# Performance work log

Measured on AMD Instinct MI355X. Metric: run time of the kernel, lower is better.

## Reference

```python
import jax, jax.numpy as jnp
import numpy as np
import math

D_MODEL = 1024
N_HEADS = 8
D_FF = 4 * D_MODEL
EPS = 1e-5


def layer_norm(x, g, b):
    mu = jnp.mean(x, axis=-1, keepdims=True)
    var = jnp.mean(jnp.square(x - mu), axis=-1, keepdims=True)
    return (x - mu) / jnp.sqrt(var + EPS) * g + b


def setup_inputs() -> dict:
    key = jax.random.key(0)
    ks = jax.random.split(key, 8)
    B, S = 1, 4096
    x = jax.random.normal(ks[0], (B, S, D_MODEL), dtype=jnp.float32)
    # linear params (stored as [in, out]); init scale ~ 1/sqrt(fan_in)
    qkv_w = jax.random.normal(ks[1], (D_MODEL, 3 * D_MODEL), dtype=jnp.float32) * (1.0 / math.sqrt(D_MODEL))
    qkv_b = jnp.zeros((3 * D_MODEL,), dtype=jnp.float32)
    w1 = jax.random.normal(ks[2], (D_MODEL, D_FF), dtype=jnp.float32) * (1.0 / math.sqrt(D_MODEL))
    b1 = jnp.zeros((D_FF,), dtype=jnp.float32)
    w2 = jax.random.normal(ks[3], (D_FF, D_MODEL), dtype=jnp.float32) * (1.0 / math.sqrt(D_FF))
    b2 = jnp.zeros((D_MODEL,), dtype=jnp.float32)
    ln1_g = jnp.ones((D_MODEL,), dtype=jnp.float32)
    ln1_b = jnp.zeros((D_MODEL,), dtype=jnp.float32)
    ln2_g = jnp.ones((D_MODEL,), dtype=jnp.float32)
    ln2_b = jnp.zeros((D_MODEL,), dtype=jnp.float32)
    return {"x": x, "ln1_g": ln1_g, "ln1_b": ln1_b, "qkv_w": qkv_w, "qkv_b": qkv_b,
            "ln2_g": ln2_g, "ln2_b": ln2_b, "w1": w1, "b1": b1, "w2": w2, "b2": b2}


def reference(x, ln1_g, ln1_b, qkv_w, qkv_b, ln2_g, ln2_b, w1, b1, w2, b2):
    B, S, D = x.shape
    hd = D // N_HEADS
    scaler = math.sqrt(hd)

    h = layer_norm(x, ln1_g, ln1_b)                       # [B,S,D]
    qkv = h @ qkv_w + qkv_b                               # [B,S,3D]
    q, k, v = jnp.split(qkv, 3, axis=-1)
    # b s (h d) -> b h s d
    def split_heads(t):
        return t.reshape(B, S, N_HEADS, hd).transpose(0, 2, 1, 3)
    q, k, v = split_heads(q), split_heads(k), split_heads(v)
    scores = jnp.einsum('bhqd,bhkd->bhqk', q, k) / scaler  # [B,H,S,S] materialized, as in source
    attn = jax.nn.softmax(scores, axis=-1)
    heads = jnp.einsum('bhqk,bhkd->bhqd', attn, v)        # [B,H,S,hd]
    attn_score = heads.transpose(0, 2, 1, 3).reshape(B, S, D)  # b h t d -> b t (h d)
    # NOTE: source returns attn_score (the proj Linear output is discarded)
    h = attn_score + h                                     # residual with ln1 output
    h = layer_norm(h, ln2_g, ln2_b)
    h = jax.nn.gelu(h @ w1 + b1, approximate=False) @ w2 + b2  # no final residual
    return h
```

## Files before the change

### kernel.cpp

```cpp
#include <hip/hip_runtime.h>
#include <stdint.h>


typedef __bf16 bf16;
typedef __attribute__((ext_vector_type(8))) __bf16 bf16x8;
typedef __attribute__((ext_vector_type(4))) __bf16 bf16x4;
typedef __attribute__((ext_vector_type(4))) float f32x4;

#define DEV static __device__ __forceinline__

#define QSCALE 0.12751741687f

DEV void gload_lds16(const void* gsrc, void* ldst) {
  typedef const __attribute__((address_space(1))) uint32_t gq_t;
  typedef __attribute__((address_space(3))) uint32_t lq_t;
  __builtin_amdgcn_global_load_lds((gq_t*)(uintptr_t)gsrc, (lq_t*)(uintptr_t)ldst,
                                   16, 0, 0);
}

DEV f32x4 mfma16(bf16x8 a, bf16x8 b, f32x4 c) {
  return __builtin_amdgcn_mfma_f32_16x16x32_bf16(a, b, c, 0, 0, 0);
}

__global__ __launch_bounds__(256) void ln1_kernel(
    const float* __restrict__ x, const float* __restrict__ gw,
    const float* __restrict__ bw, bf16* __restrict__ out) {
  int row = blockIdx.x, t = threadIdx.x;
  const float* xr = x + (size_t)row * 1024;
  f32x4 v = *(const f32x4*)(xr + t * 4);
  float s = v[0] + v[1] + v[2] + v[3];
  float s2 = v[0] * v[0] + v[1] * v[1] + v[2] * v[2] + v[3] * v[3];
#pragma unroll
  for (int off = 1; off < 64; off <<= 1) {
    s += __shfl_xor(s, off);
    s2 += __shfl_xor(s2, off);
  }
  __shared__ float red[8];
  if ((t & 63) == 0) { red[t >> 6] = s; red[4 + (t >> 6)] = s2; }
  __syncthreads();
  s = red[0] + red[1] + red[2] + red[3];
  s2 = red[4] + red[5] + red[6] + red[7];
  float mu = s * (1.f / 1024.f);
  float rstd = rsqrtf(s2 * (1.f / 1024.f) - mu * mu + 1e-5f);
  f32x4 gv = *(const f32x4*)(gw + t * 4);
  f32x4 bv = *(const f32x4*)(bw + t * 4);
  bf16x4 o;
#pragma unroll
  for (int j = 0; j < 4; j++) o[j] = (bf16)((v[j] - mu) * rstd * gv[j] + bv[j]);
  *(bf16x4*)(out + (size_t)row * 1024 + t * 4) = o;
}

__global__ __launch_bounds__(256) void resid_ln2_kernel(
    const bf16* __restrict__ Op, const float* __restrict__ lbuf,
    const bf16* __restrict__ h, const float* __restrict__ gw,
    const float* __restrict__ bw, bf16* __restrict__ out) {
  int row = blockIdx.x, t = threadIdx.x;
  int head = t >> 5;
  float l = 0.f;
  float acc[4] = {0.f, 0.f, 0.f, 0.f};
#pragma unroll
  for (int z = 0; z < 4; z++) {
    l += lbuf[(size_t)(z * 8 + head) * 4096 + row];
    bf16x4 ov = *(const bf16x4*)(Op + (size_t)z * 4096 * 1024 +
                                 (size_t)row * 1024 + t * 4);
#pragma unroll
    for (int j = 0; j < 4; j++) acc[j] += (float)ov[j];
  }
  float rl = 1.0f / l;
  bf16x4 hv = *(const bf16x4*)(h + (size_t)row * 1024 + t * 4);
  float vv[4];
#pragma unroll
  for (int j = 0; j < 4; j++) vv[j] = acc[j] * rl + (float)hv[j];
  float s = vv[0] + vv[1] + vv[2] + vv[3];
  float s2 = vv[0] * vv[0] + vv[1] * vv[1] + vv[2] * vv[2] + vv[3] * vv[3];
#pragma unroll
  for (int off = 1; off < 64; off <<= 1) {
    s += __shfl_xor(s, off);
    s2 += __shfl_xor(s2, off);
  }
  __shared__ float red[8];
  if ((t & 63) == 0) { red[t >> 6] = s; red[4 + (t >> 6)] = s2; }
  __syncthreads();
  s = red[0] + red[1] + red[2] + red[3];
  s2 = red[4] + red[5] + red[6] + red[7];
  float mu = s * (1.f / 1024.f);
  float rstd = rsqrtf(s2 * (1.f / 1024.f) - mu * mu + 1e-5f);
  f32x4 gv = *(const f32x4*)(gw + t * 4);
  f32x4 bv = *(const f32x4*)(bw + t * 4);
  bf16x4 o;
#pragma unroll
  for (int j = 0; j < 4; j++) o[j] = (bf16)((vv[j] - mu) * rstd * gv[j] + bv[j]);
  *(bf16x4*)(out + (size_t)row * 1024 + t * 4) = o;
}

__global__ __launch_bounds__(256) void ffn2_combine_kernel(
    const bf16* __restrict__ P, const float* __restrict__ b2,
    float* __restrict__ out) {
  int row = blockIdx.x, t = threadIdx.x;
  float acc[4];
  f32x4 bv = *(const f32x4*)(b2 + t * 4);
#pragma unroll
  for (int j = 0; j < 4; j++) acc[j] = bv[j];
#pragma unroll
  for (int z = 0; z < 4; z++) {
    bf16x4 pv = *(const bf16x4*)(P + (size_t)z * 4096 * 1024 +
                                 (size_t)row * 1024 + t * 4);
#pragma unroll
    for (int j = 0; j < 4; j++) acc[j] += (float)pv[j];
  }
  f32x4 o = {acc[0], acc[1], acc[2], acc[3]};
  *(f32x4*)(out + (size_t)row * 1024 + t * 4) = o;
}

__global__ __launch_bounds__(256) void transpose_f32_bf16(
    const float* __restrict__ in, bf16* __restrict__ out, int R, int C) {
  __shared__ float tile[32][33];
  int c0 = blockIdx.x * 32, r0 = blockIdx.y * 32;
  int tx = threadIdx.x & 31, ty = threadIdx.x >> 5;
#pragma unroll
  for (int j = 0; j < 4; j++)
    tile[ty + 8 * j][tx] = in[(size_t)(r0 + ty + 8 * j) * C + c0 + tx];
  __syncthreads();
#pragma unroll
  for (int j = 0; j < 4; j++)
    out[(size_t)(c0 + ty + 8 * j) * R + r0 + tx] = (bf16)tile[tx][ty + 8 * j];
}

template <int EPILOG>
__global__ __launch_bounds__(512) void gemm8p_kernel(
    const bf16* __restrict__ A, const bf16* __restrict__ Bt,
    const float* __restrict__ bias, bf16* __restrict__ Cout,
    bf16* __restrict__ Vout, int M, int N, int K, int Ks) {
  extern __shared__ char smem[];
  if constexpr (EPILOG == 4) {
    size_t zo = (size_t)blockIdx.z * Ks;
    A += zo; Bt += zo;
    Cout += (size_t)blockIdx.z * ((size_t)M * N);
  }
  int nwg = gridDim.x * gridDim.y;
  int bid = blockIdx.y * gridDim.x + blockIdx.x;
  int swz = (bid & 7) * (nwg >> 3) + (bid >> 3);
  int bx = swz % gridDim.x, by = swz / gridDim.x;
  int m0 = by * 256, n0 = bx * 256;
  int tid = threadIdx.x, wave = tid >> 6, lane = tid & 63;
  int lr = lane & 15, lg = lane >> 4;
  int wr = (wave >> 2) * 128;
  int wc = (wave & 3) * 64;
  const int NT = Ks >> 6;

  f32x4 acc[8][4] = {};

  const int sArow = tid >> 3;
  const int scbA = ((tid & 7) * 16) ^ (((tid >> 3) & 7) << 4);
  const int scbB = ((lane & 7) * 16) ^ ((lane >> 3) << 4);

  auto stageA = [&](int c, int T) {
    char* sAb = smem + (size_t)(T & 1) * 32768;
#pragma unroll
    for (int j = 0; j < 2; j++) {
      int r0 = j * 128 + 64 * c;
      gload_lds16(A + (size_t)(m0 + r0 + sArow) * K + T * 64 + scbA / 2,
                  sAb + r0 * 128 + wave * 1024);
    }
  };
  auto stageB = [&](int c, int T) {
    char* sBb = smem + 65536 + (size_t)(T & 1) * 32768;
    int wrun = (wave >> 2) * 64 + 32 * c + (wave & 3) * 8;
#pragma unroll
    for (int j = 0; j < 2; j++) {
      int r0 = j * 128 + wrun;
      gload_lds16(Bt + (size_t)(n0 + r0 + (lane >> 3)) * K + T * 64 + scbB / 2,
                  sBb + r0 * 128);
    }
  };
  auto ldA = [&](bf16x8 (&af)[4][2], int qm, int b) {
    const char* sAb = smem + (size_t)b * 32768;
#pragma unroll
    for (int mm = 0; mm < 4; mm++)
#pragma unroll
      for (int kk = 0; kk < 2; kk++) {
        int rl = wr + 64 * qm + mm * 16 + lr;
        int db = (kk * 64 + lg * 16) ^ ((rl & 7) << 4);
        af[mm][kk] = *(const bf16x8*)(sAb + rl * 128 + db);
      }
  };
  auto ldB = [&](bf16x8 (&bfv)[2][2], int qn, int b) {
    const char* sBb = smem + 65536 + (size_t)b * 32768;
#pragma unroll
    for (int nn = 0; nn < 2; nn++)
#pragma unroll
      for (int kk = 0; kk < 2; kk++) {
        int rb = wc + 32 * qn + nn * 16 + lr;
        int db = (kk * 64 + lg * 16) ^ ((rb & 7) << 4);
        bfv[nn][kk] = *(const bf16x8*)(sBb + rb * 128 + db);
      }
  };
  auto mfmaQ = [&](bf16x8 (&af)[4][2], bf16x8 (&bfv)[2][2], int qm, int qn) {
    __builtin_amdgcn_s_setprio(1);
#pragma unroll
    for (int kk = 0; kk < 2; kk++)
#pragma unroll
      for (int mm = 0; mm < 4; mm++)
#pragma unroll
        for (int nn = 0; nn < 2; nn++)
          acc[qm * 4 + mm][qn * 2 + nn] =
              mfma16(af[mm][kk], bfv[nn][kk], acc[qm * 4 + mm][qn * 2 + nn]);
    __builtin_amdgcn_s_setprio(0);
  };

  stageA(0, 0); stageB(0, 0); stageA(1, 0); stageB(1, 0);
  stageA(0, 1); stageB(0, 1);
  asm volatile("s_waitcnt vmcnt(4)" ::: "memory");
  __builtin_amdgcn_s_barrier();

  for (int T = 0; T < NT; T++) {
    int b = T & 1;
    bf16x8 af[4][2], bfv[2][2];
    ldA(af, 0, b); ldB(bfv, 0, b);
    if (T + 1 < NT) stageA(1, T + 1);
    __builtin_amdgcn_s_barrier();
    mfmaQ(af, bfv, 0, 0);
    __builtin_amdgcn_s_barrier();
    ldB(bfv, 1, b);
    if (T + 1 < NT) stageB(1, T + 1);
    __builtin_amdgcn_s_barrier();
    mfmaQ(af, bfv, 0, 1);
    __builtin_amdgcn_s_barrier();
    ldA(af, 1, b); ldB(bfv, 0, b);
    if (T + 2 < NT) stageA(0, T + 2);
    __builtin_amdgcn_s_barrier();
    mfmaQ(af, bfv, 1, 0);
    __builtin_amdgcn_s_barrier();
    ldB(bfv, 1, b);
    if (T + 2 < NT) stageB(0, T + 2);
    __builtin_amdgcn_s_barrier();
    mfmaQ(af, bfv, 1, 1);
    if (T < NT - 2) asm volatile("s_waitcnt vmcnt(4)" ::: "memory");
    else            asm volatile("s_waitcnt vmcnt(0)" ::: "memory");
    __builtin_amdgcn_s_barrier();
  }

#pragma unroll
  for (int n = 0; n < 4; n++) {
    int col = n0 + wc + n * 16 + lr;
    float bs = (EPILOG == 4) ? 0.f : bias[col];
#pragma unroll
    for (int m = 0; m < 8; m++) {
      int row0 = m0 + wr + m * 16 + lg * 4;
      if constexpr (EPILOG == 3) {
        if (col >= 2048) {
          bf16x4 pk;
#pragma unroll
          for (int r = 0; r < 4; r++) pk[r] = (bf16)(acc[m][n][r] + bs);
          *(bf16x4*)(Vout + (size_t)(col - 2048) * 4096 + row0) = pk;
          continue;
        }
      }
#pragma unroll
      for (int r = 0; r < 4; r++) {
        float v = acc[m][n][r] + bs;
        if constexpr (EPILOG == 1) {
          float u = v + 0.044715f * v * v * v;
          float e = __builtin_amdgcn_exp2f(-2.3021144f * u);
          v = v / (1.0f + e);
        }
        if constexpr (EPILOG == 3) { if (col < 1024) v *= QSCALE; }
        Cout[(size_t)(row0 + r) * N + col] = (bf16)v;
      }
    }
  }
}

__global__ __launch_bounds__(256) void attn_kernel(
    const bf16* __restrict__ qkv, const bf16* __restrict__ vt,
    bf16* __restrict__ opart, float* __restrict__ lbuf) {
  constexpr int S = 4096, C3 = 3072;
  __shared__ bf16 sK[64 * 128];
  __shared__ bf16 sV[128 * 64];
  __shared__ bf16 sP[4 * 32 * 64];
  int hh = blockIdx.y;
  int q0 = blockIdx.x * 128;
  int z = blockIdx.z;
  int kv_begin = z * (S / 4), kv_end = kv_begin + (S / 4);
  bf16* obuf = opart + (size_t)z * 4096 * 1024;
  int tid = threadIdx.x, wave = tid >> 6, lane = tid & 63;
  int lr = lane & 15, lg = lane >> 4;

  bf16x8 qf[2][4];
#pragma unroll
  for (int qs = 0; qs < 2; qs++) {
    const bf16* qrow =
        qkv + (size_t)(q0 + wave * 32 + qs * 16 + lr) * C3 + hh * 128 + lg * 8;
#pragma unroll
    for (int kk = 0; kk < 4; kk++) qf[qs][kk] = *(const bf16x8*)(qrow + kk * 32);
  }
  f32x4 o[2][8] = {};
  float lsum[2] = {0.f, 0.f};

  const int krow_s = tid >> 4;
  const int kcb = (tid & 15) * 16;
  const int scbK = kcb ^ ((krow_s & 7) << 4);
  const int vrow_s = tid >> 3;
  const int vcb = (tid & 7) * 16;
  const int scbV = vcb ^ ((vrow_s & 7) << 4);

  const bf16* kbase = qkv + 1024 + hh * 128 + scbK / 2;
  const bf16* vbase = vt + (size_t)(hh * 128 + vrow_s) * S + scbV / 2;

  for (int kv0 = kv_begin; kv0 < kv_end; kv0 += 64) {
#pragma unroll
    for (int i = 0; i < 4; i++)
      gload_lds16(kbase + (size_t)(kv0 + i * 16 + krow_s) * C3,
                  (char*)sK + i * 4096 + wave * 1024);
#pragma unroll
    for (int i = 0; i < 4; i++)
      gload_lds16(vbase + (size_t)(i * 32) * S + kv0,
                  (char*)sV + i * 4096 + wave * 1024);
    __syncthreads();

    char* pw = (char*)sP + wave * 4096;

#pragma unroll
    for (int nf = 0; nf < 4; nf++) {
      f32x4 sc0 = {0.f, 0.f, 0.f, 0.f}, sc1 = sc0;
      __builtin_amdgcn_s_setprio(1);
#pragma unroll
      for (int kk = 0; kk < 4; kk++) {
        int krow = nf * 16 + lr;
        int db = (kk * 64 + lg * 16) ^ ((krow & 7) << 4);
        bf16x8 kf = *(const bf16x8*)((const char*)sK + krow * 256 + db);
        sc0 = mfma16(kf, qf[0][kk], sc0);
        sc1 = mfma16(kf, qf[1][kk], sc1);
      }
      __builtin_amdgcn_s_setprio(0);
      f32x4 scs[2] = {sc0, sc1};
#pragma unroll
      for (int qs = 0; qs < 2; qs++) {
        float p0 = __builtin_amdgcn_exp2f(scs[qs][0]);
        float p1 = __builtin_amdgcn_exp2f(scs[qs][1]);
        float p2 = __builtin_amdgcn_exp2f(scs[qs][2]);
        float p3 = __builtin_amdgcn_exp2f(scs[qs][3]);
        lsum[qs] += (p0 + p1) + (p2 + p3);
        bf16x4 pk;
        pk[0] = (bf16)p0; pk[1] = (bf16)p1; pk[2] = (bf16)p2; pk[3] = (bf16)p3;
        *(bf16x4*)(pw + (qs * 16 + lr) * 128 +
                   ((nf * 32 + lg * 8) ^ ((lr & 7) << 4))) = pk;
      }
    }

    bf16x8 pa[2][2];
#pragma unroll
    for (int qs = 0; qs < 2; qs++)
#pragma unroll
      for (int kk = 0; kk < 2; kk++) {
        int db = (kk * 64 + lg * 16) ^ ((lr & 7) << 4);
        pa[qs][kk] = *(const bf16x8*)(pw + (qs * 16 + lr) * 128 + db);
      }
    __builtin_amdgcn_s_setprio(1);
#pragma unroll
    for (int df = 0; df < 8; df++) {
#pragma unroll
      for (int kk = 0; kk < 2; kk++) {
        int vrow = df * 16 + lr;
        int db = (kk * 64 + lg * 16) ^ ((vrow & 7) << 4);
        bf16x8 vf = *(const bf16x8*)((const char*)sV + vrow * 128 + db);
        o[0][df] = mfma16(pa[0][kk], vf, o[0][df]);
        o[1][df] = mfma16(pa[1][kk], vf, o[1][df]);
      }
    }
    __builtin_amdgcn_s_setprio(0);
    __syncthreads();
  }

#pragma unroll
  for (int qs = 0; qs < 2; qs++) {
    float ls = lsum[qs];
    ls += __shfl_xor(ls, 16);
    ls += __shfl_xor(ls, 32);
    if (lg == 0)
      lbuf[(size_t)(z * 8 + hh) * 4096 + q0 + wave * 32 + qs * 16 + lr] = ls;
#pragma unroll
    for (int df = 0; df < 8; df++) {
      int col = hh * 128 + df * 16 + lr;
#pragma unroll
      for (int r = 0; r < 4; r++) {
        int row = q0 + wave * 32 + qs * 16 + lg * 4 + r;
        obuf[(size_t)row * 1024 + col] = (bf16)o[qs][df][r];
      }
    }
  }
}

extern "C" void kernel_launch(void* const* d_in, const int* in_sizes, int n_in,
                              void* d_out, int out_size, void* d_ws, size_t ws_size,
                              hipStream_t stream) {
  const float* x     = (const float*)d_in[0];
  const float* ln1_g = (const float*)d_in[1];
  const float* ln1_b = (const float*)d_in[2];
  const float* qkv_w = (const float*)d_in[3];
  const float* qkv_b = (const float*)d_in[4];
  const float* ln2_g = (const float*)d_in[5];
  const float* ln2_b = (const float*)d_in[6];
  const float* w1    = (const float*)d_in[7];
  const float* b1    = (const float*)d_in[8];
  const float* w2    = (const float*)d_in[9];
  const float* b2    = (const float*)d_in[10];

  char* ws = (char*)d_ws;
  const size_t MB = 1ull << 20;
  bf16*  h     = (bf16*)(ws + 0);
  bf16*  qkv   = (bf16*)(ws + 8 * MB);
  bf16*  h2    = (bf16*)(ws + 8 * MB);
  bf16*  w1T   = (bf16*)(ws + 16 * MB);
  bf16*  fpart = (bf16*)(ws + 0);
  bf16*  vt    = (bf16*)(ws + 32 * MB);
  bf16*  w2T   = (bf16*)(ws + 32 * MB);
  bf16*  Op    = (bf16*)(ws + 40 * MB);
  bf16*  ffn1  = (bf16*)(ws + 40 * MB);
  float* lbuf  = (float*)(ws + 72 * MB);
  bf16*  wTq   = (bf16*)(ws + 72 * MB + 512 * 1024);
  float* outp  = (float*)d_out;

  hipFuncSetAttribute(reinterpret_cast<const void*>(gemm8p_kernel<3>),
                      hipFuncAttributeMaxDynamicSharedMemorySize, 131072);
  hipFuncSetAttribute(reinterpret_cast<const void*>(gemm8p_kernel<1>),
                      hipFuncAttributeMaxDynamicSharedMemorySize, 131072);
  hipFuncSetAttribute(reinterpret_cast<const void*>(gemm8p_kernel<4>),
                      hipFuncAttributeMaxDynamicSharedMemorySize, 131072);

  ln1_kernel<<<4096, 256, 0, stream>>>(x, ln1_g, ln1_b, h);
  transpose_f32_bf16<<<dim3(3072 / 32, 1024 / 32), 256, 0, stream>>>(qkv_w, wTq, 1024, 3072);
  gemm8p_kernel<3><<<dim3(3072 / 256, 4096 / 256), 512, 131072, stream>>>(
      h, wTq, qkv_b, qkv, vt, 4096, 3072, 1024, 1024);
  attn_kernel<<<dim3(32, 8, 4), 256, 0, stream>>>(qkv, vt, Op, lbuf);
  transpose_f32_bf16<<<dim3(4096 / 32, 1024 / 32), 256, 0, stream>>>(w1, w1T, 1024, 4096);
  transpose_f32_bf16<<<dim3(1024 / 32, 4096 / 32), 256, 0, stream>>>(w2, w2T, 4096, 1024);
  resid_ln2_kernel<<<4096, 256, 0, stream>>>(Op, lbuf, h, ln2_g, ln2_b, h2);
  gemm8p_kernel<1><<<dim3(4096 / 256, 4096 / 256), 512, 131072, stream>>>(
      h2, w1T, b1, ffn1, nullptr, 4096, 4096, 1024, 1024);
  gemm8p_kernel<4><<<dim3(1024 / 256, 4096 / 256, 4), 512, 131072, stream>>>(
      ffn1, w2T, nullptr, fpart, nullptr, 4096, 1024, 4096, 1024);
  ffn2_combine_kernel<<<4096, 256, 0, stream>>>(fpart, b2, outp);
}
```

Baseline: 249.9 us.

## Double-buffer K/V tiles in attention and merge the two FFN weight transposes

The attention kernel moves K/V staging into dynamic shared memory with two buffers, prefetching the next 64-key tile via global_load_lds while computing on the current one. This is meant to hide global-load latency that the old load-sync-compute loop exposed. LDS per block grows from about 48KB to 80KB, which may lower occupancy. The two separate w1/w2 transpose launches are also merged into one kernel to save a launch.

```diff
diff --git a/kernel.cpp b/kernel.cpp
--- a/kernel.cpp
+++ b/kernel.cpp
@@ -112,6 +112,30 @@
   *(f32x4*)(out + (size_t)row * 1024 + t * 4) = o;
 }
 
+__global__ __launch_bounds__(256) void transpose2_kernel(
+    const float* __restrict__ w1, bf16* __restrict__ w1T,
+    const float* __restrict__ w2, bf16* __restrict__ w2T) {
+  __shared__ float tile[32][33];
+  int bid = blockIdx.x;
+  const float* in; bf16* out; int R, C, c0, r0;
+  if (bid < 4096) {
+    in = w1; out = w1T; R = 1024; C = 4096;
+    c0 = (bid & 127) * 32; r0 = (bid >> 7) * 32;
+  } else {
+    int idx = bid - 4096;
+    in = w2; out = w2T; R = 4096; C = 1024;
+    c0 = (idx & 31) * 32; r0 = (idx >> 5) * 32;
+  }
+  int tx = threadIdx.x & 31, ty = threadIdx.x >> 5;
+#pragma unroll
+  for (int j = 0; j < 4; j++)
+    tile[ty + 8 * j][tx] = in[(size_t)(r0 + ty + 8 * j) * C + c0 + tx];
+  __syncthreads();
+#pragma unroll
+  for (int j = 0; j < 4; j++)
+    out[(size_t)(c0 + ty + 8 * j) * R + r0 + tx] = (bf16)tile[tx][ty + 8 * j];
+}
+
 __global__ __launch_bounds__(256) void transpose_f32_bf16(
     const float* __restrict__ in, bf16* __restrict__ out, int R, int C) {
   __shared__ float tile[32][33];
@@ -275,9 +299,7 @@
     const bf16* __restrict__ qkv, const bf16* __restrict__ vt,
     bf16* __restrict__ opart, float* __restrict__ lbuf) {
   constexpr int S = 4096, C3 = 3072;
-  __shared__ bf16 sK[64 * 128];
-  __shared__ bf16 sV[128 * 64];
-  __shared__ bf16 sP[4 * 32 * 64];
+  extern __shared__ char asmem[];
   int hh = blockIdx.y;
   int q0 = blockIdx.x * 128;
   int z = blockIdx.z;
@@ -307,18 +329,27 @@
   const bf16* kbase = qkv + 1024 + hh * 128 + scbK / 2;
   const bf16* vbase = vt + (size_t)(hh * 128 + vrow_s) * S + scbV / 2;
 
+  char* pw = asmem + 65536 + wave * 4096;
+
+#define STAGE(B, KV0)                                                        \
+  do {                                                                       \
+    _Pragma("unroll") for (int i = 0; i < 4; i++)                            \
+        gload_lds16(kbase + (size_t)((KV0) + i * 16 + krow_s) * C3,          \
+                    asmem + (B) * 16384 + i * 4096 + wave * 1024);           \
+    _Pragma("unroll") for (int i = 0; i < 4; i++)                            \
+        gload_lds16(vbase + (size_t)(i * 32) * S + (KV0),                    \
+                    asmem + 32768 + (B) * 16384 + i * 4096 + wave * 1024);   \
+  } while (0)
+
+  STAGE(0, kv_begin);
+  __syncthreads();
+  int buf = 0;
+
   for (int kv0 = kv_begin; kv0 < kv_end; kv0 += 64) {
-#pragma unroll
-    for (int i = 0; i < 4; i++)
-      gload_lds16(kbase + (size_t)(kv0 + i * 16 + krow_s) * C3,
-                  (char*)sK + i * 4096 + wave * 1024);
-#pragma unroll
-    for (int i = 0; i < 4; i++)
-      gload_lds16(vbase + (size_t)(i * 32) * S + kv0,
-                  (char*)sV + i * 4096 + wave * 1024);
-    __syncthreads();
-
-    char* pw = (char*)sP + wave * 4096;
+    if (kv0 + 64 < kv_end) STAGE(buf ^ 1, kv0 + 64);
+
+    const char* sKb = asmem + buf * 16384;
+    const char* sVb = asmem + 32768 + buf * 16384;
 
 #pragma unroll
     for (int nf = 0; nf < 4; nf++) {
@@ -328,7 +359,7 @@
       for (int kk = 0; kk < 4; kk++) {
         int krow = nf * 16 + lr;
         int db = (kk * 64 + lg * 16) ^ ((krow & 7) << 4);
-        bf16x8 kf = *(const bf16x8*)((const char*)sK + krow * 256 + db);
+        bf16x8 kf = *(const bf16x8*)(sKb + krow * 256 + db);
         sc0 = mfma16(kf, qf[0][kk], sc0);
         sc1 = mfma16(kf, qf[1][kk], sc1);
       }
@@ -363,14 +394,16 @@
       for (int kk = 0; kk < 2; kk++) {
         int vrow = df * 16 + lr;
         int db = (kk * 64 + lg * 16) ^ ((vrow & 7) << 4);
-        bf16x8 vf = *(const bf16x8*)((const char*)sV + vrow * 128 + db);
+        bf16x8 vf = *(const bf16x8*)(sVb + vrow * 128 + db);
         o[0][df] = mfma16(pa[0][kk], vf, o[0][df]);
         o[1][df] = mfma16(pa[1][kk], vf, o[1][df]);
       }
     }
     __builtin_amdgcn_s_setprio(0);
     __syncthreads();
-  }
+    buf ^= 1;
+  }
+#undef STAGE
 
 #pragma unroll
   for (int qs = 0; qs < 2; qs++) {
@@ -427,14 +460,15 @@
                       hipFuncAttributeMaxDynamicSharedMemorySize, 131072);
   hipFuncSetAttribute(reinterpret_cast<const void*>(gemm8p_kernel<4>),
                       hipFuncAttributeMaxDynamicSharedMemorySize, 131072);
+  hipFuncSetAttribute(reinterpret_cast<const void*>(attn_kernel),
+                      hipFuncAttributeMaxDynamicSharedMemorySize, 81920);
 
   ln1_kernel<<<4096, 256, 0, stream>>>(x, ln1_g, ln1_b, h);
   transpose_f32_bf16<<<dim3(3072 / 32, 1024 / 32), 256, 0, stream>>>(qkv_w, wTq, 1024, 3072);
   gemm8p_kernel<3><<<dim3(3072 / 256, 4096 / 256), 512, 131072, stream>>>(
       h, wTq, qkv_b, qkv, vt, 4096, 3072, 1024, 1024);
-  attn_kernel<<<dim3(32, 8, 4), 256, 0, stream>>>(qkv, vt, Op, lbuf);
-  transpose_f32_bf16<<<dim3(4096 / 32, 1024 / 32), 256, 0, stream>>>(w1, w1T, 1024, 4096);
-  transpose_f32_bf16<<<dim3(1024 / 32, 4096 / 32), 256, 0, stream>>>(w2, w2T, 4096, 1024);
+  attn_kernel<<<dim3(32, 8, 4), 256, 81920, stream>>>(qkv, vt, Op, lbuf);
+  transpose2_kernel<<<8192, 256, 0, stream>>>(w1, w1T, w2, w2T);
   resid_ln2_kernel<<<4096, 256, 0, stream>>>(Op, lbuf, h, ln2_g, ln2_b, h2);
   gemm8p_kernel<1><<<dim3(4096 / 256, 4096 / 256), 512, 131072, stream>>>(
       h2, w1T, b1, ffn1, nullptr, 4096, 4096, 1024, 1024);
```

New measurement: 244.1 us. 2.3% less time.
